# Kernel tuning notes

Hardware: AMD Instinct MI355X
Metric: run time of the kernel (lower is better)

Reference implementation:

```python
import jax, jax.numpy as jnp
import numpy as np

NEG_BIG = -1e10


def setup_inputs() -> dict:
    key = jax.random.key(0)
    k1, k2, k3 = jax.random.split(key, 3)
    B, C, S, H = 4, 32, 64, 256
    inputs = jax.random.normal(k1, (B, C, S, H), dtype=jnp.float32)
    mask = jnp.ones((B, C, S), dtype=jnp.float32)
    att_self = jax.random.uniform(k2, (B, C, S), dtype=jnp.float32)
    W = jax.random.normal(k3, (H, H), dtype=jnp.float32) * (1.0 / np.sqrt(H))
    return {"inputs": inputs, "mask": mask, "att_self": att_self, "W": W}


def reference(inputs, mask, att_self, W):
    # inputs: [B, C, S, H]; mask, att_self: [B, C, S]; W: [H, H] (linear1, no bias)
    # linear1(inputs2): x @ W^T applied to the query-side copy
    proj = jnp.einsum('bish,gh->bisg', inputs, W)          # [B, C, S, H]
    # scores[b,i,j,s,t] = proj[b,i,s,:] . inputs[b,j,t,:]
    scores = jnp.einsum('bish,bjth->bijst', proj, inputs)  # [B, C, C, S, S]
    # additive mask depends on (j, t) only (key side), broadcast over i and s
    scores = scores + (1.0 - mask)[:, None, :, None, :] * NEG_BIG
    # torch code computes softmax then overwrites with sigmoid -> sigmoid is effective
    att = jax.nn.sigmoid(scores)                            # [B, C, C, S, S]
    ctx = jnp.einsum('bijst,bjth->bijsh', att, inputs)      # [B, C, C, S, H]
    # selfatt weights over s (query sentence tokens), indexed by i
    fused = jnp.einsum('bis,bijsh->bijh', att_self, ctx)    # [B, C, C, H]
    return (fused, att)
```

## Files before the change

kernel.cpp:

```cpp
#include <hip/hip_runtime.h>
#include <hip/hip_bf16.h>

typedef __bf16 bf16x8 __attribute__((ext_vector_type(8)));
typedef float  f32x4  __attribute__((ext_vector_type(4)));
typedef float  f32x16 __attribute__((ext_vector_type(16)));

#define NEG_BIG (-1e10f)

constexpr int FUSED_N = 4 * 32 * 32 * 256;


__device__ __forceinline__ void async_ld16(const void* g, void* l) {
    __builtin_amdgcn_global_load_lds(
        (const __attribute__((address_space(1))) void*)g,
        (__attribute__((address_space(3))) void*)l, 16, 0, 0);
}

__device__ __forceinline__ int swzp(int row, int g) {
    return (row * 32 + (g ^ row)) * 8;
}

__global__ __launch_bounds__(256) void convw_kernel(
    const float* __restrict__ W, __bf16* __restrict__ Wh, __bf16* __restrict__ Wl) {
    int idx = blockIdx.x * 256 + threadIdx.x;
    float4 v = ((const float4*)W)[idx];
    float f[4] = {v.x, v.y, v.z, v.w};
    union { __bf16 b[4]; uint2 u; } H, L;
#pragma unroll
    for (int k = 0; k < 4; ++k) {
        __bf16 h = (__bf16)f[k];
        H.b[k] = h;
        L.b[k] = (__bf16)(f[k] - (float)h);
    }
    *(uint2*)&Wh[idx * 4] = H.u;
    *(uint2*)&Wl[idx * 4] = L.u;
}

__global__ __launch_bounds__(256, 2) void prep_kernel(
    const float* __restrict__ Xf,
    const __bf16* __restrict__ Wh, const __bf16* __restrict__ Wl,
    __bf16* __restrict__ XhG, __bf16* __restrict__ XlG,
    __bf16* __restrict__ Ph, __bf16* __restrict__ Pl) {
    __shared__ __align__(16) __bf16 sXh[16 * 256];
    __shared__ __align__(16) __bf16 sXl[16 * 256];
    const int tid = threadIdx.x, rb = blockIdx.x;

#pragma unroll
    for (int it = 0; it < 2; ++it) {
        int idx = it * 256 + tid;
        int row = idx >> 5, g = idx & 31;
        const float* p = Xf + (rb * 16 + row) * 256 + g * 8;
        float4 v0 = *(const float4*)p;
        float4 v1 = *(const float4*)(p + 4);
        float f[8] = {v0.x, v0.y, v0.z, v0.w, v1.x, v1.y, v1.z, v1.w};
        union { __bf16 b[8]; uint4 u; } H, L;
#pragma unroll
        for (int k = 0; k < 8; ++k) {
            __bf16 h = (__bf16)f[k];
            H.b[k] = h;
            L.b[k] = (__bf16)(f[k] - (float)h);
        }
        int go = (rb * 16 + row) * 256 + g * 8;
        *(uint4*)&XhG[go] = H.u;
        *(uint4*)&XlG[go] = L.u;
        int o = swzp(row, g);
        *(uint4*)&sXh[o] = H.u;
        *(uint4*)&sXl[o] = L.u;
    }
    __syncthreads();

    const int lane = tid & 63, wave = tid >> 6, m = lane & 15, quad = lane >> 4;
    bf16x8 Ah[8], Al[8];
#pragma unroll
    for (int k0 = 0; k0 < 8; ++k0) {
        int o = swzp(m, k0 * 4 + quad);
        Ah[k0] = *(const bf16x8*)&sXh[o];
        Al[k0] = *(const bf16x8*)&sXl[o];
    }
    f32x4 acc[4];
    const f32x4 z = {0.f, 0.f, 0.f, 0.f};
#pragma unroll
    for (int n = 0; n < 4; ++n) acc[n] = z;
#pragma unroll
    for (int k0 = 0; k0 < 8; ++k0) {
#pragma unroll
        for (int n = 0; n < 4; ++n) {
            const int gcol = wave * 64 + n * 16 + m;
            const int wo = gcol * 256 + k0 * 32 + quad * 8;
            bf16x8 bh = *(const bf16x8*)&Wh[wo];
            bf16x8 bl = *(const bf16x8*)&Wl[wo];
            acc[n] = __builtin_amdgcn_mfma_f32_16x16x32_bf16(Ah[k0], bh, acc[n], 0, 0, 0);
            acc[n] = __builtin_amdgcn_mfma_f32_16x16x32_bf16(Ah[k0], bl, acc[n], 0, 0, 0);
            acc[n] = __builtin_amdgcn_mfma_f32_16x16x32_bf16(Al[k0], bh, acc[n], 0, 0, 0);
        }
    }
#pragma unroll
    for (int n = 0; n < 4; ++n)
#pragma unroll
        for (int r = 0; r < 4; ++r) {
            int row = rb * 16 + quad * 4 + r;
            int col = wave * 64 + n * 16 + m;
            float v = acc[n][r];
            __bf16 h = (__bf16)v;
            Ph[row * 256 + col] = h;
            Pl[row * 256 + col] = (__bf16)(v - (float)h);
        }
}

__global__ __launch_bounds__(512, 4) void main_kernel(
    const float* __restrict__ Xf, const float* __restrict__ maskf,
    const float* __restrict__ aselff,
    const __bf16* __restrict__ XhG, const __bf16* __restrict__ XlG,
    const __bf16* __restrict__ PhG, const __bf16* __restrict__ PlG,
    float* __restrict__ out) {
    __shared__ __align__(16) __bf16 sPh[64 * 256];
    __shared__ __align__(16) __bf16 sPl[64 * 256];
    __shared__ float sW[8][64];
    __shared__ float sAs[64];
    const int tid = threadIdx.x;
    const int jq = blockIdx.x & 3;
    const int i  = (blockIdx.x >> 2) & 31;
    const int b  = blockIdx.x >> 7;
    const int lane = tid & 63, wave = tid >> 6;
    const int c31 = lane & 31, hi = lane >> 5, m15 = lane & 15;

    const int pbase = (b * 32 + i) * 16384;
    {
        const int rowhalf = lane >> 5;
        const int gslot = lane & 31;
#pragma unroll
        for (int it = 0; it < 4; ++it) {
            const int insti = wave * 4 + it;
            const int row = insti * 2 + rowhalf;
            const int g = gslot ^ (row & 15);
            const int src = pbase + row * 256 + g * 8;
            async_ld16(&PhG[src], &sPh[insti * 512]);
            async_ld16(&PlG[src], &sPl[insti * 512]);
        }
    }

    if (tid < 64) sAs[tid] = aselff[(b * 32 + i) * 64 + tid];

    __syncthreads();

    const int j = jq * 8 + wave;
    const int xb = (b * 32 + j) * 16384;

    const int boff = xb + c31 * 256 + hi * 8;
    const int arow0 = c31 * 256;
    const int arow1 = (32 + c31) * 256;

    f32x16 acc00, acc01, acc10, acc11;
#pragma unroll
    for (int e = 0; e < 16; ++e) { acc00[e] = 0.f; acc01[e] = 0.f; acc10[e] = 0.f; acc11[e] = 0.f; }

#pragma unroll
    for (int kc = 0; kc < 16; ++kc) {
        bf16x8 Bh0 = *(const bf16x8*)&XhG[boff + kc * 16];
        bf16x8 Bh1 = *(const bf16x8*)&XhG[boff + 32 * 256 + kc * 16];
        bf16x8 Bl0 = *(const bf16x8*)&XlG[boff + kc * 16];
        bf16x8 Bl1 = *(const bf16x8*)&XlG[boff + 32 * 256 + kc * 16];
        const int slot = ((kc * 2 + hi) ^ m15) * 8;
        bf16x8 Ah0 = *(const bf16x8*)&sPh[arow0 + slot];
        bf16x8 Ah1 = *(const bf16x8*)&sPh[arow1 + slot];
        bf16x8 Al0 = *(const bf16x8*)&sPl[arow0 + slot];
        bf16x8 Al1 = *(const bf16x8*)&sPl[arow1 + slot];

        acc00 = __builtin_amdgcn_mfma_f32_32x32x16_bf16(Ah0, Bh0, acc00, 0, 0, 0);
        acc00 = __builtin_amdgcn_mfma_f32_32x32x16_bf16(Ah0, Bl0, acc00, 0, 0, 0);
        acc00 = __builtin_amdgcn_mfma_f32_32x32x16_bf16(Al0, Bh0, acc00, 0, 0, 0);
        acc01 = __builtin_amdgcn_mfma_f32_32x32x16_bf16(Ah0, Bh1, acc01, 0, 0, 0);
        acc01 = __builtin_amdgcn_mfma_f32_32x32x16_bf16(Ah0, Bl1, acc01, 0, 0, 0);
        acc01 = __builtin_amdgcn_mfma_f32_32x32x16_bf16(Al0, Bh1, acc01, 0, 0, 0);
        acc10 = __builtin_amdgcn_mfma_f32_32x32x16_bf16(Ah1, Bh0, acc10, 0, 0, 0);
        acc10 = __builtin_amdgcn_mfma_f32_32x32x16_bf16(Ah1, Bl0, acc10, 0, 0, 0);
        acc10 = __builtin_amdgcn_mfma_f32_32x32x16_bf16(Al1, Bh0, acc10, 0, 0, 0);
        acc11 = __builtin_amdgcn_mfma_f32_32x32x16_bf16(Ah1, Bh1, acc11, 0, 0, 0);
        acc11 = __builtin_amdgcn_mfma_f32_32x32x16_bf16(Ah1, Bl1, acc11, 0, 0, 0);
        acc11 = __builtin_amdgcn_mfma_f32_32x32x16_bf16(Al1, Bh1, acc11, 0, 0, 0);
    }

    const float* mrow = maskf + (b * 32 + j) * 64;
    float madd[2];
#pragma unroll
    for (int ng = 0; ng < 2; ++ng)
        madd[ng] = (1.0f - mrow[ng * 32 + c31]) * NEG_BIG;

    float part[2] = {0.f, 0.f};
    float* outA = out + FUSED_N + ((size_t)((b * 32 + i) * 32 + j)) * 4096;
#pragma unroll
    for (int rg = 0; rg < 2; ++rg)
#pragma unroll
        for (int r = 0; r < 16; ++r) {
            const int s = rg * 32 + (r & 3) + 8 * (r >> 2) + 4 * hi;
            const float as_ = sAs[s];
            const float a0v = (rg == 0) ? acc00[r] : acc10[r];
            const float a1v = (rg == 0) ? acc01[r] : acc11[r];
            {
                float x = a0v + madd[0];
                float a = 1.0f / (1.0f + __expf(-x));
                outA[s * 64 + c31] = a;
                part[0] += as_ * a;
            }
            {
                float x = a1v + madd[1];
                float a = 1.0f / (1.0f + __expf(-x));
                outA[s * 64 + 32 + c31] = a;
                part[1] += as_ * a;
            }
        }
    part[0] += __shfl_xor(part[0], 32, 64);
    part[1] += __shfl_xor(part[1], 32, 64);
    if (hi == 0) {
        sW[wave][c31] = part[0];
        sW[wave][32 + c31] = part[1];
    }
    const float* Xg = Xf + xb;
    float4 acf = {0.f, 0.f, 0.f, 0.f};
#pragma unroll 8
    for (int t = 0; t < 64; ++t) {
        const float wv = sW[wave][t];
        float4 xv = *(const float4*)&Xg[t * 256 + lane * 4];
        acf.x += wv * xv.x;
        acf.y += wv * xv.y;
        acf.z += wv * xv.z;
        acf.w += wv * xv.w;
    }
    *(float4*)&out[((size_t)((b * 32 + i) * 32 + j)) * 256 + lane * 4] = acf;
}

extern "C" void kernel_launch(void* const* d_in, const int* in_sizes, int n_in,
                              void* d_out, int out_size, void* d_ws, size_t ws_size,
                              hipStream_t stream) {
    const float* X     = (const float*)d_in[0];
    const float* mask  = (const float*)d_in[1];
    const float* aself = (const float*)d_in[2];
    const float* W     = (const float*)d_in[3];
    float* out = (float*)d_out;

    __bf16* ws = (__bf16*)d_ws;
    const size_t NX = 2097152, NW = 65536;
    __bf16* Xh = ws;
    __bf16* Xl = Xh + NX;
    __bf16* Ph = Xl + NX;
    __bf16* Pl = Ph + NX;
    __bf16* Wh = Pl + NX;
    __bf16* Wl = Wh + NW;

    convw_kernel<<<dim3(64), dim3(256), 0, stream>>>(W, Wh, Wl);
    prep_kernel<<<dim3(512), dim3(256), 0, stream>>>(X, Wh, Wl, Xh, Xl, Ph, Pl);
    main_kernel<<<dim3(512), dim3(512), 0, stream>>>(
        X, mask, aself, Xh, Xl, Ph, Pl, out);
}
```

Before: 149.5 us.

## Split fused weighted-sum into separate kernel reusing X rows across queries

The main kernel no longer computes the final fused output inline. It now writes the per-(b,i,j) weight vectors over t to a workspace buffer. A new kernel, one block per (b,j) and half of H, loads the weights for all 32 i and reads each X[b,j] row once, accumulating 32 outputs per thread. This removes the repeated fp32 reads of X[b,j] that each (b,i) block used to make, at the cost of an extra launch, a global round-trip for the weights, and strided output stores.

```diff
diff --git a/kernel.cpp b/kernel.cpp
--- a/kernel.cpp
+++ b/kernel.cpp
@@ -108,14 +108,12 @@
 }
 
 __global__ __launch_bounds__(512, 4) void main_kernel(
-    const float* __restrict__ Xf, const float* __restrict__ maskf,
-    const float* __restrict__ aselff,
+    const float* __restrict__ maskf, const float* __restrict__ aselff,
     const __bf16* __restrict__ XhG, const __bf16* __restrict__ XlG,
     const __bf16* __restrict__ PhG, const __bf16* __restrict__ PlG,
-    float* __restrict__ out) {
+    float* __restrict__ wW, float* __restrict__ out) {
     __shared__ __align__(16) __bf16 sPh[64 * 256];
     __shared__ __align__(16) __bf16 sPl[64 * 256];
-    __shared__ float sW[8][64];
     __shared__ float sAs[64];
     const int tid = threadIdx.x;
     const int jq = blockIdx.x & 3;
@@ -212,21 +210,43 @@
     part[0] += __shfl_xor(part[0], 32, 64);
     part[1] += __shfl_xor(part[1], 32, 64);
     if (hi == 0) {
-        sW[wave][c31] = part[0];
-        sW[wave][32 + c31] = part[1];
-    }
-    const float* Xg = Xf + xb;
-    float4 acf = {0.f, 0.f, 0.f, 0.f};
+        float* wg = wW + ((size_t)((b * 32 + i) * 32 + j)) * 64;
+        wg[c31] = part[0];
+        wg[32 + c31] = part[1];
+    }
+}
+
+__global__ __launch_bounds__(128) void fused_kernel(
+    const float* __restrict__ Xf, const float* __restrict__ wW,
+    float* __restrict__ out) {
+    __shared__ float sw[32][64];
+    const int bj = blockIdx.x >> 1;
+    const int hh = blockIdx.x & 1;
+    const int tid = threadIdx.x;
+    const int b = bj >> 5, j = bj & 31;
+
+#pragma unroll
+    for (int k = 0; k < 16; ++k) {
+        const int idx = k * 128 + tid;
+        const int ii = idx >> 6, t = idx & 63;
+        sw[ii][t] = wW[((size_t)(b * 1024 + ii * 32 + j)) * 64 + t];
+    }
+    __syncthreads();
+
+    const int h = hh * 128 + tid;
+    const float* Xg = Xf + (size_t)bj * 16384 + h;
+    float acc[32];
+#pragma unroll
+    for (int ii = 0; ii < 32; ++ii) acc[ii] = 0.f;
 #pragma unroll 8
     for (int t = 0; t < 64; ++t) {
-        const float wv = sW[wave][t];
-        float4 xv = *(const float4*)&Xg[t * 256 + lane * 4];
-        acf.x += wv * xv.x;
-        acf.y += wv * xv.y;
-        acf.z += wv * xv.z;
-        acf.w += wv * xv.w;
-    }
-    *(float4*)&out[((size_t)((b * 32 + i) * 32 + j)) * 256 + lane * 4] = acf;
+        const float xv = Xg[t * 256];
+#pragma unroll
+        for (int ii = 0; ii < 32; ++ii) acc[ii] += sw[ii][t] * xv;
+    }
+    float* og = out + (size_t)(b * 1024 + j) * 256 + h;
+#pragma unroll
+    for (int ii = 0; ii < 32; ++ii) og[(size_t)ii * 8192] = acc[ii];
 }
 
 extern "C" void kernel_launch(void* const* d_in, const int* in_sizes, int n_in,
@@ -246,9 +266,11 @@
     __bf16* Pl = Ph + NX;
     __bf16* Wh = Pl + NX;
     __bf16* Wl = Wh + NW;
+    float*  wW = (float*)(Wl + NW);
 
     convw_kernel<<<dim3(64), dim3(256), 0, stream>>>(W, Wh, Wl);
     prep_kernel<<<dim3(512), dim3(256), 0, stream>>>(X, Wh, Wl, Xh, Xl, Ph, Pl);
     main_kernel<<<dim3(512), dim3(512), 0, stream>>>(
-        X, mask, aself, Xh, Xl, Ph, Pl, out);
-}
+        mask, aself, Xh, Xl, Ph, Pl, wW, out);
+    fused_kernel<<<dim3(256), dim3(128), 0, stream>>>(X, wW, out);
+}
```

After: 171.2 us. 14.5% more time.
